# Kernel optimization log

Hardware: AMD Instinct MI355X
Metric: run time of the kernel (lower is better)

## Reference

```python
import jax, jax.numpy as jnp
import numpy as np
from jax import lax

DN = ('NCHW', 'OIHW', 'NCHW')

def binarize(w):
    # torch: w.sign().add(0.5).sign() maps w<0 -> -1, w>=0 -> +1 (0 -> +1)
    return jnp.where(w < 0, -1.0, 1.0).astype(w.dtype)

def bconv(x, w, b, dil):
    wb = binarize(w)
    y = lax.conv_general_dilated(x, wb, window_strides=(1, 1), padding='SAME',
                                 rhs_dilation=dil, dimension_numbers=DN)
    return y + b[None, :, None, None]

def setup_inputs() -> dict:
    key = jax.random.key(0)
    ks = jax.random.split(key, 9)
    C = 256
    Co = C // 4
    x = jax.random.normal(ks[0], (16, C, 128, 128), dtype=jnp.float32)
    w1 = jax.random.normal(ks[1], (Co, C, 1, 5), dtype=jnp.float32) * 0.05
    w2 = jax.random.normal(ks[2], (Co, C, 1, 5), dtype=jnp.float32) * 0.05
    w3 = jax.random.normal(ks[3], (Co, C, 5, 1), dtype=jnp.float32) * 0.05
    w4 = jax.random.normal(ks[4], (Co, C, 5, 1), dtype=jnp.float32) * 0.05
    b1 = jax.random.normal(ks[5], (Co,), dtype=jnp.float32) * 0.01
    b2 = jax.random.normal(ks[6], (Co,), dtype=jnp.float32) * 0.01
    b3 = jax.random.normal(ks[7], (Co,), dtype=jnp.float32) * 0.01
    b4 = jax.random.normal(ks[8], (Co,), dtype=jnp.float32) * 0.01
    return {'x': x, 'w1': w1, 'b1': b1, 'w2': w2, 'b2': b2,
            'w3': w3, 'b3': b3, 'w4': w4, 'b4': b4}

def reference(x, w1, b1, w2, b2, w3, b3, w4, b4):
    out1 = bconv(x, w1, b1, (1, 1))  # (1,5) dil 1
    out2 = bconv(x, w2, b2, (2, 2))  # (1,5) dil 2 (only W dim matters, H kernel=1)
    out3 = bconv(x, w3, b3, (1, 1))  # (5,1) dil 1
    out4 = bconv(x, w4, b4, (2, 2))  # (5,1) dil 2
    return jnp.concatenate([out1, out2, out3, out4], axis=1)
```

## Files before the change

### kernel.cpp

```cpp
#include <hip/hip_runtime.h>

typedef _Float16 half8   __attribute__((ext_vector_type(8)));
typedef float    floatx4 __attribute__((ext_vector_type(4)));
typedef unsigned int uint4v __attribute__((ext_vector_type(4)));

#define HW      128
#define CIN     256
#define NCHUNK  8
#define HALO_W  24
#define HALO_H  16
#define NPIX    (HALO_W * HALO_H)
#define PITCH   20

__global__ void prep_weights(const float* __restrict__ w1,
                             const float* __restrict__ w2,
                             const float* __restrict__ w3,
                             const float* __restrict__ w4,
                             _Float16* __restrict__ wp)
{
    int idx  = blockIdx.x * 256 + threadIdx.x;
    int j    = idx & 7;
    int lane = (idx >> 3) & 63;
    int m    = (idx >> 9) & 3;
    int r3   = idx >> 11;
    int t    = r3 % 5;
    int r4   = r3 / 5;
    int chunk= r4 & 7;
    int b    = r4 >> 3;
    const float* w = (b == 0) ? w1 : (b == 1) ? w2 : (b == 2) ? w3 : w4;
    int co = m * 16 + (lane & 15);
    int ci = chunk * 32 + (lane >> 4) * 8 + j;
    float v = w[(co * 256 + ci) * 5 + t];
    wp[idx] = (v < 0.0f) ? (_Float16)(-1.0f) : (_Float16)(1.0f);
}

__global__ __launch_bounds__(256, 2)
void bconv_mfma(const float* __restrict__ x,
                const _Float16* __restrict__ wp,
                const float* __restrict__ bb1,
                const float* __restrict__ bb2,
                const float* __restrict__ bb3,
                const float* __restrict__ bb4,
                float* __restrict__ out)
{
    __shared__ __align__(16) unsigned int xs[2 * NPIX * PITCH];
    __shared__ float bias_s[256];

    const int tid  = threadIdx.x;
    const int w0t  = blockIdx.x * 16;
    const int h0t  = blockIdx.y * 8;
    const int nimg = blockIdx.z;

    {
        int br = tid >> 6, i = tid & 63;
        const float* bp = (br == 0) ? bb1 : (br == 1) ? bb2 : (br == 2) ? bb3 : bb4;
        bias_s[tid] = bp[i];
    }

    const int lane = tid & 63;
    const int wave = tid >> 6;
    const int quad = lane >> 4;
    const int wl   = lane & 15;
    const int dil  = (wave & 1) + 1;
    const bool horiz = (wave < 2);

    floatx4 acc[4][8];
    #pragma unroll
    for (int m = 0; m < 4; ++m)
        #pragma unroll
        for (int n = 0; n < 8; ++n)
            acc[m][n] = (floatx4){0.f, 0.f, 0.f, 0.f};

    auto stage = [&](int buf, int chunk) {
        unsigned int* xb = &xs[buf * (NPIX * PITCH)];
        #pragma unroll
        for (int s = 0; s < 6; ++s) {
            int idx = s * 256 + tid;
            int hh  = idx / 96;
            int rem = idx - hh * 96;
            int cb  = rem / 24;
            int ww  = rem - cb * 24;
            int hg  = h0t - 4 + hh;
            int wg  = w0t - 4 + ww;
            float v[8];
            #pragma unroll
            for (int jj = 0; jj < 8; ++jj) v[jj] = 0.0f;
            if (hg >= 0 && hg < HW && wg >= 0 && wg < HW) {
                const float* p = x + (((nimg * CIN + chunk * 32 + cb * 8) * HW + hg) * HW + wg);
                #pragma unroll
                for (int jj = 0; jj < 8; ++jj) v[jj] = p[jj * HW * HW];
            }
            uint4v u;
            #pragma unroll
            for (int jj = 0; jj < 4; ++jj)
                u[jj] = __builtin_bit_cast(unsigned int,
                            __builtin_amdgcn_cvt_pkrtz(v[2 * jj], v[2 * jj + 1]));
            *(uint4v*)&xb[(hh * HALO_W + ww) * PITCH + cb * 4] = u;
        }
    };

    stage(0, 0);

    for (int k = 0; k < NCHUNK; ++k) {
        __syncthreads();
        const unsigned int* xb  = &xs[(k & 1) * (NPIX * PITCH)];
        const _Float16*     wpc = wp + (wave * 8 + k) * (5 * 4 * 64 * 8);

        #pragma unroll
        for (int t = 0; t < 5; ++t) {
            half8 B[8];
            #pragma unroll
            for (int n = 0; n < 8; ++n) {
                int hh, ww;
                if (horiz) { hh = n + 4;                  ww = wl + 4 + (t - 2) * dil; }
                else       { hh = n + 4 + (t - 2) * dil;  ww = wl + 4; }
                B[n] = *(const half8*)&xb[(hh * HALO_W + ww) * PITCH + quad * 4];
            }
            #pragma unroll
            for (int m = 0; m < 4; ++m) {
                half8 A = *(const half8*)(wpc + ((t * 4 + m) * 64 + lane) * 8);
                #pragma unroll
                for (int n = 0; n < 8; ++n)
                    acc[m][n] = __builtin_amdgcn_mfma_f32_16x16x32_f16(A, B[n], acc[m][n], 0, 0, 0);
            }
        }

        if (k + 1 < NCHUNK) stage((k + 1) & 1, k + 1);
    }

    float bv[4][4];
    #pragma unroll
    for (int m = 0; m < 4; ++m)
        #pragma unroll
        for (int r = 0; r < 4; ++r)
            bv[m][r] = bias_s[wave * 64 + m * 16 + quad * 4 + r];

    #pragma unroll
    for (int m = 0; m < 4; ++m) {
        #pragma unroll
        for (int n = 0; n < 8; ++n) {
            int co   = wave * 64 + m * 16 + quad * 4;
            int base = ((nimg * 256 + co) * HW + (h0t + n)) * HW + w0t + wl;
            #pragma unroll
            for (int r = 0; r < 4; ++r)
                out[base + r * HW * HW] = acc[m][n][r] + bv[m][r];
        }
    }
}

extern "C" void kernel_launch(void* const* d_in, const int* in_sizes, int n_in,
                              void* d_out, int out_size, void* d_ws, size_t ws_size,
                              hipStream_t stream)
{
    (void)in_sizes; (void)n_in; (void)out_size; (void)ws_size;
    const float* x  = (const float*)d_in[0];
    const float* w1 = (const float*)d_in[1];
    const float* b1 = (const float*)d_in[2];
    const float* w2 = (const float*)d_in[3];
    const float* b2 = (const float*)d_in[4];
    const float* w3 = (const float*)d_in[5];
    const float* b3 = (const float*)d_in[6];
    const float* w4 = (const float*)d_in[7];
    const float* b4 = (const float*)d_in[8];
    float*    out = (float*)d_out;
    _Float16* wp  = (_Float16*)d_ws;

    prep_weights<<<1280, 256, 0, stream>>>(w1, w2, w3, w4, wp);

    dim3 grid(128 / 16, 128 / 8, 16);
    bconv_mfma<<<grid, dim3(256), 0, stream>>>(x, wp, b1, b2, b3, b4, out);
}
```

Baseline: 660.8 us.

## Prefetch next input chunk into registers to overlap global loads with MFMA

```diff
diff --git a/kernel.cpp b/kernel.cpp
--- a/kernel.cpp
+++ b/kernel.cpp
@@ -71,37 +71,53 @@
         for (int n = 0; n < 8; ++n)
             acc[m][n] = (floatx4){0.f, 0.f, 0.f, 0.f};
 
-    auto stage = [&](int buf, int chunk) {
+    int s_hh[6], s_ww[6], s_cb[6];
+    bool s_ok[6];
+    #pragma unroll
+    for (int s = 0; s < 6; ++s) {
+        int idx = s * 256 + tid;
+        int hh  = idx / 96;
+        int rem = idx - hh * 96;
+        int cb  = rem / 24;
+        int ww  = rem - cb * 24;
+        s_hh[s] = hh; s_ww[s] = ww; s_cb[s] = cb;
+        int hg = h0t - 4 + hh;
+        int wg = w0t - 4 + ww;
+        s_ok[s] = (hg >= 0 && hg < HW && wg >= 0 && wg < HW);
+    }
+
+    float vreg[6][8];
+
+    auto stage_load = [&](int chunk) {
+        #pragma unroll
+        for (int s = 0; s < 6; ++s) {
+            int hg = h0t - 4 + s_hh[s];
+            int wg = w0t - 4 + s_ww[s];
+            const float* p = x + (((nimg * CIN + chunk * 32 + s_cb[s] * 8) * HW + hg) * HW + wg);
+            #pragma unroll
+            for (int jj = 0; jj < 8; ++jj)
+                vreg[s][jj] = s_ok[s] ? p[jj * HW * HW] : 0.0f;
+        }
+    };
+
+    auto stage_write = [&](int buf) {
         unsigned int* xb = &xs[buf * (NPIX * PITCH)];
         #pragma unroll
         for (int s = 0; s < 6; ++s) {
-            int idx = s * 256 + tid;
-            int hh  = idx / 96;
-            int rem = idx - hh * 96;
-            int cb  = rem / 24;
-            int ww  = rem - cb * 24;
-            int hg  = h0t - 4 + hh;
-            int wg  = w0t - 4 + ww;
-            float v[8];
-            #pragma unroll
-            for (int jj = 0; jj < 8; ++jj) v[jj] = 0.0f;
-            if (hg >= 0 && hg < HW && wg >= 0 && wg < HW) {
-                const float* p = x + (((nimg * CIN + chunk * 32 + cb * 8) * HW + hg) * HW + wg);
-                #pragma unroll
-                for (int jj = 0; jj < 8; ++jj) v[jj] = p[jj * HW * HW];
-            }
             uint4v u;
             #pragma unroll
             for (int jj = 0; jj < 4; ++jj)
                 u[jj] = __builtin_bit_cast(unsigned int,
-                            __builtin_amdgcn_cvt_pkrtz(v[2 * jj], v[2 * jj + 1]));
-            *(uint4v*)&xb[(hh * HALO_W + ww) * PITCH + cb * 4] = u;
+                            __builtin_amdgcn_cvt_pkrtz(vreg[s][2 * jj], vreg[s][2 * jj + 1]));
+            *(uint4v*)&xb[(s_hh[s] * HALO_W + s_ww[s]) * PITCH + s_cb[s] * 4] = u;
         }
     };
 
-    stage(0, 0);
+    stage_load(0);
 
     for (int k = 0; k < NCHUNK; ++k) {
+        stage_write(k & 1);
+        if (k + 1 < NCHUNK) stage_load(k + 1);
         __syncthreads();
         const unsigned int* xb  = &xs[(k & 1) * (NPIX * PITCH)];
         const _Float16*     wpc = wp + (wave * 8 + k) * (5 * 4 * 64 * 8);
@@ -124,8 +140,6 @@
                     acc[m][n] = __builtin_amdgcn_mfma_f32_16x16x32_f16(A, B[n], acc[m][n], 0, 0, 0);
             }
         }
-
-        if (k + 1 < NCHUNK) stage((k + 1) & 1, k + 1);
     }
 
     float bv[4][4];
```

Result: slower. 1.312 ms (+98.6%).
